# Kernel tuning notes

Measured on AMD Instinct MI355X. Metric: run time of the kernel, lower is better.

## Reference

```python
import jax, jax.numpy as jnp
from jax import lax
import numpy as np

B, NG, NC = 4, 513, 512  # batch, grid size N, coef size N-1

_STENCILS = [[[-1/6, 2/3], [-1/3, -1/6]],
             [[2/3, -1/6], [-1/6, -1/3]],
             [[-1/6, -1/3], [2/3, -1/6]],
             [[-1/3, -1/6], [-1/6, 2/3]]]

def _kernel():
    # torch: vstack 4 (1,1,2,2) kernels -> permute(1,0,2,3) => (out=1, in=4, 2, 2)
    return jnp.asarray(_STENCILS, jnp.float32)[None]

def darcy(x, a, kernel):
    # x: (B,1,N,N), a: (B,1,N-1,N-1)
    N = x.shape[-1]
    X = jnp.concatenate([x[:, :, 1:N, :N-1] * a,
                         x[:, :, 1:N, 1:] * a,
                         x[:, :, :N-1, 1:] * a,
                         x[:, :, :N-1, :N-1] * a], axis=1)  # (B,4,N-1,N-1)
    Ax = lax.conv_general_dilated(X, kernel, (1, 1), 'VALID')  # (B,1,N-2,N-2)
    return jnp.pad(Ax, ((0, 0), (0, 0), (1, 1), (1, 1)))

def _conv3(x, w):
    # x: (Cin,H,W), w: (Cout,Cin,3,3), padding=1
    return lax.conv_general_dilated(x[None], w, (1, 1), ((1, 1), (1, 1)))[0]
_CONVB = jax.vmap(_conv3)

def mcc(x, w):
    # per-sample complex 3x3 conv == torch multi_channel_conv diagonal trick
    yr = _CONVB(x.real, w.real) - _CONVB(x.imag, w.imag)
    yi = _CONVB(x.real, w.imag) + _CONVB(x.imag, w.real)
    return yr + 1j * yi

def conjT(w):
    # transpose(-4,-3).transpose(-2,-1).conj()
    return jnp.conj(jnp.swapaxes(jnp.swapaxes(w, 1, 2), -2, -1))

def expand(r):
    Bb, C, M, N = r.shape
    Z = jnp.zeros((Bb, C, 2 * (M + 1), 2 * (N + 1)), r.dtype)
    Z = Z.at[:, :, 1:M+1, 1:N+1].set(r)
    Z = Z.at[:, :, M+2:, 1:N+1].set(-r[:, :, ::-1, :])
    Z = Z.at[:, :, 1:M+1, N+2:].set(-r[:, :, :, ::-1])
    Z = Z.at[:, :, M+2:, N+2:].set(r[:, :, ::-1, ::-1])
    kg = jnp.arange(-M - 1, N + 1, dtype=jnp.float32) * jnp.float32(np.pi)
    ik2 = 1.0 / (kg[:, None] ** 2 + kg[None, :] ** 2)
    ik2 = ik2.at[M + 1, N + 1].set(1.0)
    N2 = 2 * (N + 1)
    lo = N2 // 2 - N2 // 4
    hi = N2 // 2 + N2 // 4 + 1
    return Z, ik2[lo:hi, lo:hi][None, None]

def H_apply(r, w1, w2, w3, wt):
    N1 = r.shape[-1]
    rsym, ik2 = expand(r)
    N2 = rsym.shape[-1]
    lo = N2 // 2 - N2 // 4
    hi = N2 // 2 + N2 // 4 + 1
    rh = jnp.fft.fftshift(jnp.fft.ifft2(rsym, axes=(2, 3)), axes=(2, 3))[:, :, lo:hi, lo:hi]
    for w in (w1, w2, w3):
        rh = mcc(rh, w)
    out = rh * wt * ik2
    for w in (conjT(w3), conjT(w2), conjT(w1)):
        out = mcc(out, w)
    pl = N2 // 4 + 1
    pr = N2 - N2 // 2 - pl
    out = jnp.pad(out, ((0, 0), (0, 0), (pl, pr), (pl, pr)))
    e = jnp.fft.fft2(jnp.fft.ifftshift(out, axes=(2, 3)), axes=(2, 3)).real
    return e[:, :, :N1, :N1]

def fns_step(x, f, a, dinv, kernel, ws):
    # Jacobi smoother, w=3/4, M=10
    for _ in range(10):
        r = f - darcy(x, a, kernel)
        x = x.at[:, :, 1:-1, 1:-1].add(0.75 * dinv * r[:, :, 1:-1, 1:-1])
    r = f - darcy(x, a, kernel)
    e = H_apply(r[:, :, 1:-1, 1:-1], *ws)
    e = jnp.pad(e, ((0, 0), (0, 0), (1, 1), (1, 1)))
    Ae = darcy(e, a, kernel)
    alpha = (jnp.sum(r * e, axis=(1, 2, 3)) / jnp.sum(Ae * e, axis=(1, 2, 3)))[:, None, None, None]
    return x + alpha * e

def _forward(f, coef, w1, w2, w3, wt, K):
    kernel = _kernel()
    diag_k = (2.0 / 3.0) * jnp.ones((1, 1, 2, 2), jnp.float32)
    dinv = 1.0 / lax.conv_general_dilated(coef, diag_k, (1, 1), 'VALID')
    ws = (w1, w2, w3, wt)
    x = jnp.zeros_like(f)
    for _ in range(K):
        x = fns_step(x, f, coef, dinv, kernel, ws)
    r = f - darcy(x, coef, kernel)
    return jnp.linalg.norm(r.reshape(-1)) / jnp.linalg.norm(f.reshape(-1))

def setup_inputs():
    key = jax.random.key(0)
    ks = jax.random.split(key, 12)
    s = jnp.float32(0.1)
    inp = {
        'f': jax.random.normal(ks[0], (B, 1, NG, NG), jnp.float32),
        'coef': jax.random.uniform(ks[1], (B, 1, NC, NC), jnp.float32) + 0.1,
        'u': jnp.zeros((B, 1, NG, NG), jnp.float32),
        'w1r': jax.random.normal(ks[2], (B, 4, 1, 3, 3), jnp.float32) * s,
        'w1i': jax.random.normal(ks[3], (B, 4, 1, 3, 3), jnp.float32) * s,
        'w2r': jax.random.normal(ks[4], (B, 4, 4, 3, 3), jnp.float32) * s,
        'w2i': jax.random.normal(ks[5], (B, 4, 4, 3, 3), jnp.float32) * s,
        'w3r': jax.random.normal(ks[6], (B, 1, 4, 3, 3), jnp.float32) * s,
        'w3i': jax.random.normal(ks[7], (B, 1, 4, 3, 3), jnp.float32) * s,
        'wtr': jax.random.normal(ks[8], (B, 1, NG, NG), jnp.float32) * s,
        'wti': jax.random.normal(ks[9], (B, 1, NG, NG), jnp.float32) * s,
        'epoch': 101,
    }
    return inp

def reference(f, coef, u, w1r, w1i, w2r, w2i, w3r, w3i, wtr, wti, epoch):
    K = (epoch - 1) // 100 + 1
    w1 = w1r + 1j * w1i
    w2 = w2r + 1j * w2i
    w3 = w3r + 1j * w3i
    wt = wtr + 1j * wti
    return _forward(f, coef, w1, w2, w3, wt, K)
```

## Files before the change

kernel.cpp:

```cpp
#include <hip/hip_runtime.h>
#include <math.h>

#ifndef M_PI
#define M_PI 3.14159265358979323846
#endif

#define NGRID 513
#define NCELL 512
#define NINT  511
#define NB    4

constexpr int N2G = NGRID * NGRID;
constexpr int NI2 = NINT * NINT;
constexpr int NTT = NGRID * NINT;

typedef unsigned short ushort;
typedef unsigned int uint32;
typedef __attribute__((ext_vector_type(8))) short short8;
typedef __attribute__((ext_vector_type(8))) unsigned short ushort8;
typedef __attribute__((ext_vector_type(4))) float f32x4;

__device__ __forceinline__ ushort f2bf(float x) {
    unsigned u = __float_as_uint(x);
    unsigned r = u + 0x7FFFu + ((u >> 16) & 1u);
    return (ushort)(r >> 16);
}
__device__ __forceinline__ float bf2f(ushort h) {
    return __uint_as_float(((unsigned)h) << 16);
}

__device__ __forceinline__ float darcyA(const float* __restrict__ x,
                                        const float* __restrict__ a,
                                        int i, int j) {
    const float c23 = 2.0f / 3.0f, c16 = 1.0f / 6.0f, c13 = 1.0f / 3.0f;
    float a00 = a[(i - 1) * NCELL + (j - 1)];
    float a01 = a[(i - 1) * NCELL + j];
    float a10 = a[i * NCELL + (j - 1)];
    float a11 = a[i * NCELL + j];
    const float* xm = x + (i - 1) * NGRID;
    const float* xc = x + i * NGRID;
    const float* xp = x + (i + 1) * NGRID;
    return c23 * (a00 + a01 + a10 + a11) * xc[j]
         - c16 * ((a00 + a01) * xm[j] + (a10 + a11) * xp[j]
                + (a00 + a10) * xc[j - 1] + (a01 + a11) * xc[j + 1])
         - c13 * (a00 * xm[j - 1] + a01 * xm[j + 1]
                + a10 * xp[j - 1] + a11 * xp[j + 1]);
}

__global__ void k_stencil(const float* __restrict__ xin,
                          const float* __restrict__ a,
                          const float* __restrict__ f,
                          const float* __restrict__ dinv,
                          float* __restrict__ out, int mode) {
    int b = blockIdx.z;
    int j = blockIdx.x * 16 + threadIdx.x;
    int i = blockIdx.y * 16 + threadIdx.y;
    if (i >= NGRID || j >= NGRID) return;
    const float* xb = xin + (long long)b * N2G;
    const float* ab = a + (long long)b * NCELL * NCELL;
    long long idx = (long long)b * N2G + (long long)i * NGRID + j;
    bool interior = (i >= 1 && i <= NINT && j >= 1 && j <= NINT);
    if (!interior) {
        out[idx] = (mode == 0) ? f[idx] : 0.0f;
        return;
    }
    float Ax = darcyA(xb, ab, i, j);
    if (mode == 0) {
        out[idx] = f[idx] - Ax;
    } else {
        out[idx] = Ax;
    }
}

__global__ void k_jacobi5(const float* __restrict__ xin,
                          const float* __restrict__ a,
                          const float* __restrict__ f,
                          const float* __restrict__ dinv,
                          float* __restrict__ out) {
    __shared__ float sx[26][26];
    __shared__ float sa[25][26];
    __shared__ float sf[24][24];
    __shared__ float sd[24][24];
    __shared__ float sp[2][24][26];
    const float c23 = 2.0f / 3.0f, c16 = 1.0f / 6.0f, c13 = 1.0f / 3.0f;
    int b = blockIdx.z;
    const float* xb = xin + (long long)b * N2G;
    const float* ab = a + (long long)b * NCELL * NCELL;
    const float* fb = f + (long long)b * N2G;
    const float* db = dinv + (long long)b * NI2;
    int ox = blockIdx.x * 16, oy = blockIdx.y * 16;
    int tx = threadIdx.x, ty = threadIdx.y;
    int tid = ty * 16 + tx;

    for (int idx = tid; idx < 26 * 26; idx += 256) {
        int ly = idx / 26, lx = idx % 26;
        int gy = oy - 5 + ly, gx = ox - 5 + lx;
        bool in = (gy >= 0 && gy < NGRID && gx >= 0 && gx < NGRID);
        sx[ly][lx] = in ? xb[(long long)gy * NGRID + gx] : 0.0f;
    }
    for (int idx = tid; idx < 25 * 25; idx += 256) {
        int ly = idx / 25, lx = idx % 25;
        int gy = oy - 5 + ly, gx = ox - 5 + lx;
        bool in = (gy >= 0 && gy < NCELL && gx >= 0 && gx < NCELL);
        sa[ly][lx] = in ? ab[(long long)gy * NCELL + gx] : 0.0f;
    }
    for (int idx = tid; idx < 24 * 24; idx += 256) {
        int ly = idx / 24, lx = idx % 24;
        int gy = oy - 4 + ly, gx = ox - 4 + lx;
        bool ing = (gy >= 0 && gy < NGRID && gx >= 0 && gx < NGRID);
        bool itr = (gy >= 1 && gy <= NINT && gx >= 1 && gx <= NINT);
        sf[ly][lx] = ing ? fb[(long long)gy * NGRID + gx] : 0.0f;
        sd[ly][lx] = itr ? db[(long long)(gy - 1) * NINT + (gx - 1)] : 0.0f;
    }
    __syncthreads();

    for (int idx = tid; idx < 24 * 24; idx += 256) {
        int ly = idx / 24, lx = idx % 24;
        int gy = oy - 4 + ly, gx = ox - 4 + lx;
        float v = 0.0f;
        if (gy >= 0 && gy < NGRID && gx >= 0 && gx < NGRID) {
            float xc = sx[ly + 1][lx + 1];
            if (gy >= 1 && gy <= NINT && gx >= 1 && gx <= NINT) {
                float a00 = sa[ly][lx], a01 = sa[ly][lx + 1];
                float a10 = sa[ly + 1][lx], a11 = sa[ly + 1][lx + 1];
                float Ax = c23 * (a00 + a01 + a10 + a11) * xc
                    - c16 * ((a00 + a01) * sx[ly][lx + 1] + (a10 + a11) * sx[ly + 2][lx + 1]
                           + (a00 + a10) * sx[ly + 1][lx] + (a01 + a11) * sx[ly + 1][lx + 2])
                    - c13 * (a00 * sx[ly][lx] + a01 * sx[ly][lx + 2]
                           + a10 * sx[ly + 2][lx] + a11 * sx[ly + 2][lx + 2]);
                v = xc + 0.75f * sd[ly][lx] * (sf[ly][lx] - Ax);
            } else {
                v = xc;
            }
        }
        sp[0][ly][lx] = v;
    }
    __syncthreads();

    #pragma unroll 1
    for (int s = 2; s <= 4; ++s) {
        int sz = 24 - 2 * (s - 1);
        int cur = (s - 1) & 1, prv = s & 1;
        for (int idx = tid; idx < sz * sz; idx += 256) {
            int ly = idx / sz, lx = idx % sz;
            int gy = oy - (5 - s) + ly, gx = ox - (5 - s) + lx;
            float v = 0.0f;
            if (gy >= 0 && gy < NGRID && gx >= 0 && gx < NGRID) {
                float xc = sp[prv][ly + 1][lx + 1];
                if (gy >= 1 && gy <= NINT && gx >= 1 && gx <= NINT) {
                    int ar = ly + s - 1, ac = lx + s - 1;
                    float a00 = sa[ar][ac], a01 = sa[ar][ac + 1];
                    float a10 = sa[ar + 1][ac], a11 = sa[ar + 1][ac + 1];
                    float Ax = c23 * (a00 + a01 + a10 + a11) * xc
                        - c16 * ((a00 + a01) * sp[prv][ly][lx + 1] + (a10 + a11) * sp[prv][ly + 2][lx + 1]
                               + (a00 + a10) * sp[prv][ly + 1][lx] + (a01 + a11) * sp[prv][ly + 1][lx + 2])
                        - c13 * (a00 * sp[prv][ly][lx] + a01 * sp[prv][ly][lx + 2]
                               + a10 * sp[prv][ly + 2][lx] + a11 * sp[prv][ly + 2][lx + 2]);
                    int fr = ly + s - 1, fc = lx + s - 1;
                    v = xc + 0.75f * sd[fr][fc] * (sf[fr][fc] - Ax);
                } else {
                    v = xc;
                }
            }
            sp[cur][ly][lx] = v;
        }
        __syncthreads();
    }

    {
        int gy = oy + ty, gx = ox + tx;
        if (gy < NGRID && gx < NGRID) {
            float v;
            float xc = sp[1][ty + 1][tx + 1];
            if (gy >= 1 && gy <= NINT && gx >= 1 && gx <= NINT) {
                int ar = ty + 4, ac = tx + 4;
                float a00 = sa[ar][ac], a01 = sa[ar][ac + 1];
                float a10 = sa[ar + 1][ac], a11 = sa[ar + 1][ac + 1];
                float Ax = c23 * (a00 + a01 + a10 + a11) * xc
                    - c16 * ((a00 + a01) * sp[1][ty][tx + 1] + (a10 + a11) * sp[1][ty + 2][tx + 1]
                           + (a00 + a10) * sp[1][ty + 1][tx] + (a01 + a11) * sp[1][ty + 1][tx + 2])
                    - c13 * (a00 * sp[1][ty][tx] + a01 * sp[1][ty][tx + 2]
                           + a10 * sp[1][ty + 2][tx] + a11 * sp[1][ty + 2][tx + 2]);
                v = xc + 0.75f * sd[ty + 4][tx + 4] * (sf[ty + 4][tx + 4] - Ax);
            } else {
                v = xc;
            }
            out[(long long)b * N2G + (long long)gy * NGRID + gx] = v;
        }
    }
}

__global__ void k_dinv(const float* __restrict__ a, float* __restrict__ dinv) {
    long long idx = (long long)blockIdx.x * blockDim.x + threadIdx.x;
    if (idx >= (long long)NB * NI2) return;
    int b = (int)(idx / NI2);
    int rem = (int)(idx % NI2);
    int p = rem / NINT, q = rem % NINT;
    const float* ab = a + (long long)b * NCELL * NCELL;
    float s = ab[p * NCELL + q] + ab[p * NCELL + q + 1]
            + ab[(p + 1) * NCELL + q] + ab[(p + 1) * NCELL + q + 1];
    dinv[idx] = 1.0f / ((2.0f / 3.0f) * s);
}

__device__ __forceinline__ void wsplit(double v, ushort* Dh, ushort* Dl, int idx) {
    float vf = (float)v;
    ushort h = f2bf(vf);
    Dh[idx] = h;
    Dl[idx] = f2bf(vf - bf2f(h));
}

__global__ void k_genDSTA(ushort* __restrict__ Dh, ushort* __restrict__ Dl) {
    int idx = blockIdx.x * 256 + threadIdx.x;
    if (idx >= 513 * 512) return;
    int u = idx / 512, k = idx % 512;
    double v = 0.0;
    if (k < 511) {
        int t = ((u - 256) * (k + 1)) % 1024;
        if (t < 0) t += 1024;
        v = sin((M_PI / 512.0) * (double)t);
    }
    wsplit(v, Dh, Dl, idx);
}

__global__ void k_genDSTB(ushort* __restrict__ Dh, ushort* __restrict__ Dl) {
    int idx = blockIdx.x * 256 + threadIdx.x;
    if (idx >= 513 * 512) return;
    int v = idx / 512, k = idx % 512;
    double val = 0.0;
    if (k < 511) {
        int t = ((v - 256) * (k + 1)) % 1024;
        if (t < 0) t += 1024;
        val = sin((M_PI / 512.0) * (double)t) * (-1.0 / 262144.0);
    }
    wsplit(val, Dh, Dl, idx);
}

__global__ void k_genFA(ushort* __restrict__ Dh, ushort* __restrict__ Dl) {
    int idx = blockIdx.x * 256 + threadIdx.x;
    if (idx >= 511 * 1056) return;
    int y = idx / 1056, k = idx % 1056;
    double v = 0.0;
    if (k < 1026) {
        int m = (k < 513) ? k : (k - 513);
        long t = ((long)y * (m - 255)) % 1025;
        if (t < 0) t += 1025;
        double ang = (2.0 * M_PI / 1025.0) * (double)t;
        v = (k < 513) ? cos(ang) : -sin(ang);
    }
    wsplit(v, Dh, Dl, idx);
}

__global__ void k_genFB(ushort* __restrict__ Dh, ushort* __restrict__ Dl) {
    int idx = blockIdx.x * 256 + threadIdx.x;
    if (idx >= 1022 * 1056) return;
    int n = idx / 1056, k = idx % 1056;
    double v = 0.0;
    if (k < 1026) {
        int m = (k < 513) ? k : (k - 513);
        int y = (n < 511) ? n : (n - 511);
        long t = ((long)y * (m - 255)) % 1025;
        if (t < 0) t += 1025;
        double ang = (2.0 * M_PI / 1025.0) * (double)t;
        bool ktop = (k < 513), nleft = (n < 511);
        if (ktop && nleft)        v = cos(ang);
        else if (ktop && !nleft)  v = -sin(ang);
        else if (!ktop && nleft)  v = sin(ang);
        else                      v = cos(ang);
    }
    wsplit(v, Dh, Dl, idx);
}

__global__ void k_cvtA(const float* __restrict__ s1, const float* __restrict__ s2,
                       long long bs1, long long bs2, int ld1, int ld2, int S,
                       int M, int K, int Kp,
                       ushort* __restrict__ Dh, ushort* __restrict__ Dl) {
    int b = blockIdx.y;
    int idx = blockIdx.x * 256 + threadIdx.x;
    if (idx >= M * Kp) return;
    int m = idx / Kp, k = idx % Kp;
    float v = 0.0f;
    if (k < K)
        v = (k < S) ? s1[b * bs1 + (long long)m * ld1 + k]
                    : s2[b * bs2 + (long long)m * ld2 + (k - S)];
    long long o = (long long)b * M * Kp + idx;
    ushort h = f2bf(v);
    Dh[o] = h;
    Dl[o] = f2bf(v - bf2f(h));
}

__global__ void k_cvtBt(const float* __restrict__ s1,
                        long long bs1, int ld1,
                        int N, int K, int Kp,
                        ushort* __restrict__ Dh, ushort* __restrict__ Dl) {
    int b = blockIdx.y;
    int idx = blockIdx.x * 256 + threadIdx.x;
    if (idx >= N * Kp) return;
    int n = idx / Kp, k = idx % Kp;
    float v = 0.0f;
    if (k < K)
        v = s1[b * bs1 + (long long)k * ld1 + n];
    long long o = (long long)b * N * Kp + idx;
    ushort h = f2bf(v);
    Dh[o] = h;
    Dl[o] = f2bf(v - bf2f(h));
}

__global__ void k_redA(const float* __restrict__ P, int nsplit,
                       ushort* __restrict__ Dh, ushort* __restrict__ Dl) {
    int b = blockIdx.y;
    int idx = blockIdx.x * 256 + threadIdx.x;
    if (idx >= 513 * 512) return;
    int m = idx / 512, k = idx % 512;
    float v = 0.0f;
    if (k < 511) {
        long long base = (long long)m * 511 + k;
        #pragma unroll 4
        for (int s = 0; s < nsplit; ++s)
            v += P[((long long)b * nsplit + s) * NTT + base];
    }
    long long o = (long long)b * 513 * 512 + idx;
    ushort h = f2bf(v);
    Dh[o] = h;
    Dl[o] = f2bf(v - bf2f(h));
}

__global__ void k_redBt(const float* __restrict__ P, int nsplit,
                        ushort* __restrict__ Dh, ushort* __restrict__ Dl) {
    int b = blockIdx.y;
    int idx = blockIdx.x * 256 + threadIdx.x;
    if (idx >= 511 * 1056) return;
    int n = idx / 1056, k = idx % 1056;
    float v = 0.0f;
    if (k < 1026) {
        int row = (k < 513) ? n : (511 + n);
        int col = (k < 513) ? k : (k - 513);
        long long base = (long long)row * 513 + col;
        float acc = 0.0f;
        #pragma unroll 4
        for (int s = 0; s < nsplit; ++s)
            acc += P[((long long)b * nsplit + s) * (1022LL * 513) + base];
        v = (k < 513) ? acc : -acc;
    }
    long long o = (long long)b * 511 * 1056 + idx;
    ushort h = f2bf(v);
    Dh[o] = h;
    Dl[o] = f2bf(v - bf2f(h));
}

__global__ __launch_bounds__(256) void k_mgemm(
    const ushort* __restrict__ Ah, const ushort* __restrict__ Al, long long bsA,
    const ushort* __restrict__ Bh, const ushort* __restrict__ Bl, long long bsB,
    float* __restrict__ C, long long bsC,
    int M, int N, int Kp, int nsplit) {
    __shared__ ushort sAh[128 * 40];
    __shared__ ushort sAl[128 * 40];
    __shared__ ushort sBh[128 * 40];
    __shared__ ushort sBl[128 * 40];

    int bz = blockIdx.z, b = bz / nsplit, ks = bz % nsplit;
    int kchunk = (((Kp + nsplit - 1) / nsplit) + 31) & ~31;
    int kbeg = ks * kchunk;
    int kend = min(Kp, kbeg + kchunk);

    Ah += b * bsA; Al += b * bsA;
    Bh += b * bsB; Bl += b * bsB;
    C += ((long long)b * nsplit + ks) * bsC;

    int bm = blockIdx.y * 128, bn = blockIdx.x * 128;
    int tid = threadIdx.x;
    int wave = tid >> 6, lane = tid & 63;
    int wm = (wave >> 1) * 64, wn = (wave & 1) * 64;
    int quad = lane >> 4, l16 = lane & 15;

    f32x4 zf = {0.f, 0.f, 0.f, 0.f};
    f32x4 acc[4][4];
    #pragma unroll
    for (int i = 0; i < 4; ++i)
        #pragma unroll
        for (int j = 0; j < 4; ++j) acc[i][j] = zf;

    int srow = tid >> 2;
    int sk8 = (tid & 3) * 8;

    for (int kt = kbeg; kt < kend; kt += 32) {
        #pragma unroll
        for (int h = 0; h < 2; ++h) {
            int row = srow + 64 * h;
            ushort8 vh = {0, 0, 0, 0, 0, 0, 0, 0};
            ushort8 vl = {0, 0, 0, 0, 0, 0, 0, 0};
            int gm = bm + row;
            if (gm < M) {
                vh = *(const ushort8*)(Ah + (long long)gm * Kp + kt + sk8);
                vl = *(const ushort8*)(Al + (long long)gm * Kp + kt + sk8);
            }
            *(ushort8*)(sAh + row * 40 + sk8) = vh;
            *(ushort8*)(sAl + row * 40 + sk8) = vl;
            ushort8 wh = {0, 0, 0, 0, 0, 0, 0, 0};
            ushort8 wl = {0, 0, 0, 0, 0, 0, 0, 0};
            int gn = bn + row;
            if (gn < N) {
                wh = *(const ushort8*)(Bh + (long long)gn * Kp + kt + sk8);
                wl = *(const ushort8*)(Bl + (long long)gn * Kp + kt + sk8);
            }
            *(ushort8*)(sBh + row * 40 + sk8) = wh;
            *(ushort8*)(sBl + row * 40 + sk8) = wl;
        }
        __syncthreads();

        short8 afh[4], afl[4], bfh[4], bfl[4];
        #pragma unroll
        for (int t = 0; t < 4; ++t) {
            int ar = wm + t * 16 + l16;
            afh[t] = *(const short8*)(sAh + ar * 40 + quad * 8);
            afl[t] = *(const short8*)(sAl + ar * 40 + quad * 8);
            int br = wn + t * 16 + l16;
            bfh[t] = *(const short8*)(sBh + br * 40 + quad * 8);
            bfl[t] = *(const short8*)(sBl + br * 40 + quad * 8);
        }
        #pragma unroll
        for (int mt = 0; mt < 4; ++mt)
            #pragma unroll
            for (int nt = 0; nt < 4; ++nt) {
                acc[mt][nt] = __builtin_amdgcn_mfma_f32_16x16x32_bf16(
                    afh[mt], bfh[nt], acc[mt][nt], 0, 0, 0);
                acc[mt][nt] = __builtin_amdgcn_mfma_f32_16x16x32_bf16(
                    afh[mt], bfl[nt], acc[mt][nt], 0, 0, 0);
                acc[mt][nt] = __builtin_amdgcn_mfma_f32_16x16x32_bf16(
                    afl[mt], bfh[nt], acc[mt][nt], 0, 0, 0);
            }
        __syncthreads();
    }

    #pragma unroll
    for (int mt = 0; mt < 4; ++mt) {
        #pragma unroll
        for (int r = 0; r < 4; ++r) {
            int gm = bm + wm + mt * 16 + quad * 4 + r;
            if (gm >= M) continue;
            long long rowoff = (long long)gm * N;
            #pragma unroll
            for (int nt = 0; nt < 4; ++nt) {
                int gn = bn + wn + nt * 16 + l16;
                if (gn < N) C[rowoff + gn] = acc[mt][nt][r];
            }
        }
    }
}

__global__ void k_reduce(const float* __restrict__ Pr,
                         float* __restrict__ outR,
                         int MN, int N, int ldo, long long bsOut, int nsplit) {
    int b = blockIdx.y;
    for (int idx = blockIdx.x * 256 + threadIdx.x; idx < MN;
         idx += gridDim.x * 256) {
        float sr = 0.0f;
        #pragma unroll 4
        for (int s = 0; s < nsplit; ++s)
            sr += Pr[((long long)b * nsplit + s) * MN + idx];
        int m = idx / N, n = idx - m * N;
        outR[(long long)b * bsOut + (long long)m * ldo + n] = sr;
    }
}

__device__ __forceinline__ float2 cmul(float2 a, float2 b) {
    return make_float2(a.x * b.x - a.y * b.y, a.x * b.y + a.y * b.x);
}

__global__ void k_compose(const float* __restrict__ w1r, const float* __restrict__ w1i,
                          const float* __restrict__ w2r, const float* __restrict__ w2i,
                          const float* __restrict__ w3r, const float* __restrict__ w3i,
                          float* __restrict__ kc) {
    int chain = blockIdx.x, b = blockIdx.y;
    int tid = threadIdx.x;
    __shared__ float2 sW1[4][9], sW2[16][9], sW3[4][9], sW21[4][25];
    for (int idx = tid; idx < 36; idx += 128) {
        int c = idx / 9, s = idx % 9, p = s / 3, q = s % 3;
        if (chain == 0) {
            int i1 = b * 36 + c * 9 + p * 3 + q;
            sW1[c][s] = make_float2(w1r[i1], w1i[i1]);
            sW3[c][s] = make_float2(w3r[i1], w3i[i1]);
        } else {
            int it = b * 36 + c * 9 + q * 3 + p;
            sW1[c][s] = make_float2(w3r[it], -w3i[it]);
            sW3[c][s] = make_float2(w1r[it], -w1i[it]);
        }
    }
    for (int idx = tid; idx < 144; idx += 128) {
        int co = idx / 36, r = idx % 36, ci = r / 9, s = r % 9, p = s / 3, q = s % 3;
        int iw = (chain == 0) ? (b * 144 + co * 36 + ci * 9 + p * 3 + q)
                              : (b * 144 + ci * 36 + co * 9 + q * 3 + p);
        float iv = w2i[iw];
        sW2[co * 4 + ci][s] = make_float2(w2r[iw], (chain == 0) ? iv : -iv);
    }
    __syncthreads();
    for (int idx = tid; idx < 100; idx += 128) {
        int cm = idx / 25, r = idx % 25, di = r / 5 - 2, dj = r % 5 - 2;
        float2 acc = make_float2(0.f, 0.f);
        for (int c1 = 0; c1 < 4; ++c1)
            for (int p = 0; p < 3; ++p)
                for (int q = 0; q < 3; ++q) {
                    int ei = di - (p - 1) + 1, ej = dj - (q - 1) + 1;
                    if (ei >= 0 && ei < 3 && ej >= 0 && ej < 3) {
                        float2 t = cmul(sW2[cm * 4 + c1][p * 3 + q], sW1[c1][ei * 3 + ej]);
                        acc.x += t.x; acc.y += t.y;
                    }
                }
        sW21[cm][r] = acc;
    }
    __syncthreads();
    for (int idx = tid; idx < 49; idx += 128) {
        int di = idx / 7 - 3, dj = idx % 7 - 3;
        float2 acc = make_float2(0.f, 0.f);
        for (int cm = 0; cm < 4; ++cm)
            for (int p = 0; p < 3; ++p)
                for (int q = 0; q < 3; ++q) {
                    int ei = di - (p - 1), ej = dj - (q - 1);
                    if (ei >= -2 && ei <= 2 && ej >= -2 && ej <= 2) {
                        float2 t = cmul(sW3[cm][p * 3 + q], sW21[cm][(ei + 2) * 5 + (ej + 2)]);
                        acc.x += t.x; acc.y += t.y;
                    }
                }
        ((float2*)kc)[(b * 2 + chain) * 49 + idx] = acc;
    }
}

template <bool CPLX>
__global__ __launch_bounds__(256) void k_conv7(
    const float* __restrict__ xr, const float* __restrict__ xi,
    const float* __restrict__ kc, int chain,
    float* __restrict__ outr, float* __restrict__ outi) {
    __shared__ float2 tile[134][23];
    __shared__ float2 kt[49];
    int b = blockIdx.z;
    int tid = threadIdx.y * 16 + threadIdx.x;
    const float2* kb = (const float2*)kc + (b * 2 + chain) * 49;
    for (int idx = tid; idx < 49; idx += 256) kt[idx] = kb[idx];
    int row_base = blockIdx.y * 128 - 3;
    int col_base = blockIdx.x * 16 - 3;
    for (int idx = tid; idx < 134 * 22; idx += 256) {
        int r = idx / 22, c = idx % 22;
        int gr = row_base + r, gc = col_base + c;
        bool in = (gr >= 0 && gr < NGRID && gc >= 0 && gc < NGRID);
        long long g = (long long)b * N2G + (long long)gr * NGRID + gc;
        float vr = in ? xr[g] : 0.0f;
        float vi = (CPLX && in) ? xi[g] : 0.0f;
        tile[r][c] = make_float2(vr, vi);
    }
    __syncthreads();

    int tx = threadIdx.x, r0 = threadIdx.y * 8;
    float2 acc[8];
    #pragma unroll
    for (int r = 0; r < 8; ++r) acc[r] = make_float2(0.f, 0.f);
    #pragma unroll
    for (int t = 0; t < 7; ++t) {
        float2 kv[7];
        #pragma unroll
        for (int s = 0; s < 7; ++s) kv[s] = kt[s * 7 + t];
        #pragma unroll
        for (int rr = 0; rr < 14; ++rr) {
            float2 xv = tile[r0 + rr][tx + t];
            #pragma unroll
            for (int s = 0; s < 7; ++s) {
                int orow = rr - s;
                if (orow >= 0 && orow < 8) {
                    acc[orow].x += kv[s].x * xv.x;
                    acc[orow].y += kv[s].y * xv.x;
                    if (CPLX) {
                        acc[orow].x -= kv[s].y * xv.y;
                        acc[orow].y += kv[s].x * xv.y;
                    }
                }
            }
        }
    }
    int gc = blockIdx.x * 16 + tx;
    if (gc >= NGRID) return;
    #pragma unroll
    for (int r = 0; r < 8; ++r) {
        int gr = blockIdx.y * 128 + r0 + r;
        if (gr < NGRID) {
            long long g = (long long)b * N2G + (long long)gr * NGRID + gc;
            outr[g] = acc[r].x;
            outi[g] = acc[r].y;
        }
    }
}

template <int CHAIN>
__global__ __launch_bounds__(256) void k_ring7(
    const float* __restrict__ xr, const float* __restrict__ xi,
    const float* __restrict__ w1r, const float* __restrict__ w1i,
    const float* __restrict__ w2r, const float* __restrict__ w2i,
    const float* __restrict__ w3r, const float* __restrict__ w3i,
    float* __restrict__ outr, float* __restrict__ outi) {
    constexpr bool CPLX = (CHAIN == 1);
    __shared__ float2 W1s[4][9], W2s[16][9], W3s[4][9];
    __shared__ float2 Y[4][4][68];
    __shared__ float2 Z[4][3][66];
    int side = blockIdx.y, b = blockIdx.z;
    int u0 = blockIdx.x * 64;
    int ulo = (side < 2) ? 0 : 2;
    int uhi = (side < 2) ? (NGRID - 1) : (NGRID - 3);
    if (u0 > uhi) return;
    int tid = threadIdx.x;

    for (int idx = tid; idx < 36; idx += 256) {
        int c = idx / 9, s = idx % 9, p = s / 3, q = s % 3;
        if (CHAIN == 0) {
            int i1 = b * 36 + c * 9 + p * 3 + q;
            W1s[c][s] = make_float2(w1r[i1], w1i[i1]);
            W3s[c][s] = make_float2(w3r[i1], w3i[i1]);
        } else {
            int it = b * 36 + c * 9 + q * 3 + p;
            W1s[c][s] = make_float2(w3r[it], -w3i[it]);
            W3s[c][s] = make_float2(w1r[it], -w1i[it]);
        }
    }
    for (int idx = tid; idx < 144; idx += 256) {
        int co = idx / 36, r = idx % 36, ci = r / 9, s = r % 9, p = s / 3, q = s % 3;
        int iw = (CHAIN == 0) ? (b * 144 + co * 36 + ci * 9 + p * 3 + q)
                              : (b * 144 + ci * 36 + co * 9 + q * 3 + p);
        float iv = w2i[iw];
        W2s[co * 4 + ci][s] = make_float2(w2r[iw], (CHAIN == 0) ? iv : -iv);
    }
    __syncthreads();

    for (int idx = tid; idx < 4 * 4 * 68; idx += 256) {
        int ch = idx / (4 * 68), r = idx % (4 * 68), d = r / 68, uu = r % 68;
        int u = u0 - 2 + uu;
        float2 acc = make_float2(0.f, 0.f);
        if (u >= 0 && u < NGRID) {
            int i, j;
            if (side == 0)      { i = d;       j = u; }
            else if (side == 1) { i = 512 - d; j = u; }
            else if (side == 2) { i = u;       j = d; }
            else                { i = u;       j = 512 - d; }
            for (int p = 0; p < 3; ++p)
                for (int q = 0; q < 3; ++q) {
                    int ii = i + p - 1, jj = j + q - 1;
                    if (ii >= 0 && ii < NGRID && jj >= 0 && jj < NGRID) {
                        long long g = (long long)b * N2G + (long long)ii * NGRID + jj;
                        float vr = xr[g];
                        float vi = CPLX ? xi[g] : 0.0f;
                        float2 w = W1s[ch][p * 3 + q];
                        acc.x += w.x * vr - w.y * vi;
                        acc.y += w.x * vi + w.y * vr;
                    }
                }
        }
        Y[ch][d][uu] = acc;
    }
    __syncthreads();

    for (int idx = tid; idx < 4 * 3 * 66; idx += 256) {
        int co = idx / (3 * 66), r = idx % (3 * 66), d = r / 66, uu = r % 66;
        int u = u0 - 1 + uu;
        float2 acc = make_float2(0.f, 0.f);
        if (u >= 0 && u < NGRID) {
            for (int p = 0; p < 3; ++p)
                for (int q = 0; q < 3; ++q) {
                    int dd, du;
                    if (side == 0)      { dd = p - 1; du = q - 1; }
                    else if (side == 1) { dd = 1 - p; du = q - 1; }
                    else if (side == 2) { dd = q - 1; du = p - 1; }
                    else                { dd = 1 - q; du = p - 1; }
                    int d2 = d + dd, uy = uu + 1 + du;
                    if (d2 >= 0) {
                        for (int ci = 0; ci < 4; ++ci) {
                            float2 yv = Y[ci][d2][uy];
                            float2 w = W2s[co * 4 + ci][p * 3 + q];
                            acc.x += w.x * yv.x - w.y * yv.y;
                            acc.y += w.x * yv.y + w.y * yv.x;
                        }
                    }
                }
        }
        Z[co][d][uu] = acc;
    }
    __syncthreads();

    for (int idx = tid; idx < 128; idx += 256) {
        int d = idx / 64, uu = idx % 64;
        int u = u0 + uu;
        if (u < ulo || u > uhi) continue;
        float2 acc = make_float2(0.f, 0.f);
        for (int p = 0; p < 3; ++p)
            for (int q = 0; q < 3; ++q) {
                int dd, du;
                if (side == 0)      { dd = p - 1; du = q - 1; }
                else if (side == 1) { dd = 1 - p; du = q - 1; }
                else if (side == 2) { dd = q - 1; du = p - 1; }
                else                { dd = 1 - q; du = p - 1; }
                int d2 = d + dd, uz = uu + 1 + du;
                if (d2 >= 0) {
                    for (int ci = 0; ci < 4; ++ci) {
                        float2 zv = Z[ci][d2][uz];
                        float2 w = W3s[ci][p * 3 + q];
                        acc.x += w.x * zv.x - w.y * zv.y;
                        acc.y += w.x * zv.y + w.y * zv.x;
                    }
                }
            }
        int i, j;
        if (side == 0)      { i = d;       j = u; }
        else if (side == 1) { i = 512 - d; j = u; }
        else if (side == 2) { i = u;       j = d; }
        else                { i = u;       j = 512 - d; }
        long long g = (long long)b * N2G + (long long)i * NGRID + j;
        outr[g] = acc.x;
        outi[g] = acc.y;
    }
}

__global__ void k_scale(float* __restrict__ or_, float* __restrict__ oi_,
                        const float* __restrict__ wtr, const float* __restrict__ wti) {
    long long idx = (long long)blockIdx.x * blockDim.x + threadIdx.x;
    if (idx >= (long long)NB * N2G) return;
    int pix = (int)(idx % N2G);
    int u = pix / NGRID, v = pix % NGRID;
    int du = u - 256, dv = v - 256;
    float ik2;
    if (du == 0 && dv == 0)
        ik2 = 1.0f;
    else
        ik2 = (float)(1.0 / (9.869604401089358 * (double)(du * du + dv * dv)));
    float xr = or_[idx], xv = oi_[idx];
    float wrv = wtr[idx], wiv = wti[idx];
    or_[idx] = (xr * wrv - xv * wiv) * ik2;
    oi_[idx] = (xr * wiv + xv * wrv) * ik2;
}

__global__ void k_dot2(const float* __restrict__ r, const float* __restrict__ e,
                       const float* __restrict__ Ae, float* __restrict__ red) {
    int b = blockIdx.y;
    const float* rb = r + (long long)b * N2G;
    const float* eb = e + (long long)b * N2G;
    const float* ab = Ae + (long long)b * N2G;
    float s1 = 0.0f, s2 = 0.0f;
    for (int i = blockIdx.x * blockDim.x + threadIdx.x; i < N2G;
         i += gridDim.x * blockDim.x) {
        float ev = eb[i];
        s1 += rb[i] * ev;
        s2 += ab[i] * ev;
    }
    #pragma unroll
    for (int o = 32; o > 0; o >>= 1) {
        s1 += __shfl_down(s1, o);
        s2 += __shfl_down(s2, o);
    }
    __shared__ float l1[4], l2[4];
    int wid = threadIdx.x >> 6;
    if ((threadIdx.x & 63) == 0) { l1[wid] = s1; l2[wid] = s2; }
    __syncthreads();
    if (threadIdx.x == 0) {
        atomicAdd(&red[2 * b], l1[0] + l1[1] + l1[2] + l1[3]);
        atomicAdd(&red[2 * b + 1], l2[0] + l2[1] + l2[2] + l2[3]);
    }
}

__global__ void k_update(float* __restrict__ x, const float* __restrict__ e,
                         const float* __restrict__ red) {
    long long idx = (long long)blockIdx.x * blockDim.x + threadIdx.x;
    if (idx >= (long long)NB * N2G) return;
    int b = (int)(idx / N2G);
    float alpha = red[2 * b] / red[2 * b + 1];
    x[idx] += alpha * e[idx];
}

__global__ void k_norm(const float* __restrict__ r, const float* __restrict__ f,
                       float* __restrict__ red) {
    float s1 = 0.0f, s2 = 0.0f;
    for (long long i = (long long)blockIdx.x * blockDim.x + threadIdx.x;
         i < (long long)NB * N2G; i += (long long)gridDim.x * blockDim.x) {
        float rv = r[i], fv = f[i];
        s1 += rv * rv;
        s2 += fv * fv;
    }
    #pragma unroll
    for (int o = 32; o > 0; o >>= 1) {
        s1 += __shfl_down(s1, o);
        s2 += __shfl_down(s2, o);
    }
    __shared__ float l1[4], l2[4];
    int wid = threadIdx.x >> 6;
    if ((threadIdx.x & 63) == 0) { l1[wid] = s1; l2[wid] = s2; }
    __syncthreads();
    if (threadIdx.x == 0) {
        atomicAdd(&red[8], l1[0] + l1[1] + l1[2] + l1[3]);
        atomicAdd(&red[9], l2[0] + l2[1] + l2[2] + l2[3]);
    }
}

__global__ void k_final(const float* __restrict__ red, float* __restrict__ out) {
    out[0] = sqrtf(red[8] / red[9]);
}

extern "C" void kernel_launch(void* const* d_in, const int* in_sizes, int n_in,
                              void* d_out, int out_size, void* d_ws, size_t ws_size,
                              hipStream_t stream) {
    (void)in_sizes; (void)n_in; (void)out_size; (void)ws_size;
    const float* f    = (const float*)d_in[0];
    const float* coef = (const float*)d_in[1];
    const float* w1r  = (const float*)d_in[3];
    const float* w1i  = (const float*)d_in[4];
    const float* w2r  = (const float*)d_in[5];
    const float* w2i  = (const float*)d_in[6];
    const float* w3r  = (const float*)d_in[7];
    const float* w3i  = (const float*)d_in[8];
    const float* wtr  = (const float*)d_in[9];
    const float* wti  = (const float*)d_in[10];
    float* out = (float*)d_out;

    float* ws = (float*)d_ws;
    size_t off = 0;
    auto alloc = [&](long long n) {
        float* p = ws + off;
        off += (size_t)((n + 3) & ~3LL);
        return p;
    };
    float* x0   = alloc((long long)NB * N2G);
    float* x1   = alloc((long long)NB * N2G);
    float* rr   = alloc((long long)NB * N2G);
    float* ee   = alloc((long long)NB * N2G);
    float* rh   = alloc((long long)NB * N2G);
    float* dinv = alloc((long long)NB * NI2);
    float* c1r  = alloc((long long)NB * 4 * N2G);
    float* c1i  = alloc((long long)NB * 4 * N2G);
    float* c2r  = alloc((long long)NB * 4 * N2G);
    float* c2i  = alloc((long long)NB * 4 * N2G);
    float* pr   = c1r;
    float* or_  = alloc((long long)NB * N2G);
    float* oi_  = alloc((long long)NB * N2G);
    float* red  = alloc(16);
    ushort* sGh  = (ushort*)alloc(513 * 512 / 2);
    ushort* sGl  = (ushort*)alloc(513 * 512 / 2);
    ushort* sGth = (ushort*)alloc(513 * 512 / 2);
    ushort* sGtl = (ushort*)alloc(513 * 512 / 2);
    ushort* sFAh = (ushort*)alloc(511 * 1056 / 2);
    ushort* sFAl = (ushort*)alloc(511 * 1056 / 2);
    ushort* sFBh = (ushort*)alloc(1022 * 1056 / 2);
    ushort* sFBl = (ushort*)alloc(1022 * 1056 / 2);
    ushort* dAh  = (ushort*)alloc((long long)NB * 513 * 1056 / 2);
    ushort* dAl  = (ushort*)alloc((long long)NB * 513 * 1056 / 2);
    ushort* dBh  = (ushort*)alloc((long long)NB * 511 * 1056 / 2);
    ushort* dBl  = (ushort*)alloc((long long)NB * 511 * 1056 / 2);
    float* kcomp = alloc(NB * 2 * 49 * 2);
    float* Ae   = rh;

    dim3 blk2(16, 16);
    dim3 grdS(33, 33, NB);
    dim3 grdC(33, 5, NB);
    dim3 grdR(9, 4, NB);
    const int SP = 4;

    hipMemsetAsync(x0, 0, (size_t)NB * N2G * sizeof(float), stream);
    k_dinv<<<dim3((NB * NI2 + 255) / 256), dim3(256), 0, stream>>>(coef, dinv);
    k_genDSTA<<<dim3((513 * 512 + 255) / 256), dim3(256), 0, stream>>>(sGh, sGl);
    k_genDSTB<<<dim3((513 * 512 + 255) / 256), dim3(256), 0, stream>>>(sGth, sGtl);
    k_genFA<<<dim3((511 * 1056 + 255) / 256), dim3(256), 0, stream>>>(sFAh, sFAl);
    k_genFB<<<dim3((1022 * 1056 + 255) / 256), dim3(256), 0, stream>>>(sFBh, sFBl);
    k_compose<<<dim3(2, NB), dim3(128), 0, stream>>>(w1r, w1i, w2r, w2i, w3r, w3i, kcomp);

    float* xa = x0;
    float* xb = x1;
    for (int step = 0; step < 2; ++step) {
        for (int it = 0; it < 2; ++it) {
            k_jacobi5<<<grdS, blk2, 0, stream>>>(xa, coef, f, dinv, xb);
            float* t = xa; xa = xb; xb = t;
        }
        k_stencil<<<grdS, blk2, 0, stream>>>(xa, coef, f, nullptr, rr, 0);

        k_cvtBt<<<dim3((511 * 512 + 255) / 256, NB), dim3(256), 0, stream>>>(
            rr + NGRID + 1, N2G, NGRID, 511, 511, 512, dBh, dBl);
        k_mgemm<<<dim3(4, 5, NB * SP), dim3(256), 0, stream>>>(
            sGh, sGl, 0, dBh, dBl, (long long)511 * 512,
            pr, (long long)NTT, 513, 511, 512, SP);
        k_redA<<<dim3(1026, NB), dim3(256), 0, stream>>>(pr, SP, dAh, dAl);
        k_mgemm<<<dim3(5, 5, NB * SP), dim3(256), 0, stream>>>(
            dAh, dAl, (long long)513 * 512, sGth, sGtl, 0,
            pr, (long long)N2G, 513, 513, 512, SP);
        k_reduce<<<dim3(1024, NB), dim3(256), 0, stream>>>(
            pr, rh, N2G, NGRID, NGRID, (long long)N2G, SP);

        k_conv7<false><<<grdC, blk2, 0, stream>>>(rh, nullptr, kcomp, 0, or_, oi_);
        k_ring7<0><<<grdR, dim3(256), 0, stream>>>(
            rh, nullptr, w1r, w1i, w2r, w2i, w3r, w3i, or_, oi_);
        k_scale<<<dim3((NB * N2G + 255) / 256), dim3(256), 0, stream>>>(or_, oi_, wtr, wti);
        k_conv7<true><<<grdC, blk2, 0, stream>>>(or_, oi_, kcomp, 1, c1r, c1i);
        k_ring7<1><<<grdR, dim3(256), 0, stream>>>(
            or_, oi_, w1r, w1i, w2r, w2i, w3r, w3i, c1r, c1i);

        k_cvtA<<<dim3((513 * 1056 + 255) / 256, NB), dim3(256), 0, stream>>>(
            c1r, c1i, N2G, N2G, NGRID, NGRID, 513, 513, 1026, 1056, dAh, dAl);
        k_mgemm<<<dim3(5, 8, NB * 4), dim3(256), 0, stream>>>(
            sFBh, sFBl, 0, dAh, dAl, (long long)513 * 1056,
            pr, 1022LL * 513, 1022, 513, 1056, 4);
        k_redBt<<<dim3(2109, NB), dim3(256), 0, stream>>>(pr, 4, dBh, dBl);
        k_mgemm<<<dim3(4, 4, NB * SP), dim3(256), 0, stream>>>(
            sFAh, sFAl, 0, dBh, dBl, (long long)511 * 1056,
            pr, (long long)NI2, 511, 511, 1056, SP);
        hipMemsetAsync(ee, 0, (size_t)NB * N2G * sizeof(float), stream);
        k_reduce<<<dim3(1024, NB), dim3(256), 0, stream>>>(
            pr, ee + NGRID + 1, NI2, NINT, NGRID, (long long)N2G, SP);

        k_stencil<<<grdS, blk2, 0, stream>>>(ee, coef, nullptr, nullptr, Ae, 2);
        hipMemsetAsync(red, 0, 8 * sizeof(float), stream);
        k_dot2<<<dim3(64, NB), dim3(256), 0, stream>>>(rr, ee, Ae, red);
        k_update<<<dim3((NB * N2G + 255) / 256), dim3(256), 0, stream>>>(xa, ee, red);
    }
    k_stencil<<<grdS, blk2, 0, stream>>>(xa, coef, f, nullptr, rr, 0);
    hipMemsetAsync(red + 8, 0, 2 * sizeof(float), stream);
    k_norm<<<dim3(256), dim3(256), 0, stream>>>(rr, f, red);
    k_final<<<dim3(1), dim3(1), 0, stream>>>(red, out);
}
```

Before: 752.0 us.

## Exploit spectral odd symmetry to compute quarter transform; fuse conversions into producers

The forward spectral transform now produces only a 257x257 quadrant, and consumers rebuild the full 513x513 field from it through a sign-flipping symmetric read. This shrinks both forward GEMMs and the reduction. The bf16 hi/lo split conversion of the residual is fused into the stencil kernel through a shared-memory transpose. The wavenumber scaling and the bf16 packing of the conv outputs are fused into conv7 and ring7, which removes the separate scale and cvtA/cvtBt passes and their global round trips. The cost is extra per-element index logic and scaling work in the conv loads, plus added memsets to zero the padded bf16 buffers.

```diff
diff --git a/kernel.cpp b/kernel.cpp
--- a/kernel.cpp
+++ b/kernel.cpp
@@ -12,7 +12,7 @@
 
 constexpr int N2G = NGRID * NGRID;
 constexpr int NI2 = NINT * NINT;
-constexpr int NTT = NGRID * NINT;
+constexpr int NQ  = 257 * 257;
 
 typedef unsigned short ushort;
 typedef unsigned int uint32;
@@ -27,6 +27,25 @@
 }
 __device__ __forceinline__ float bf2f(ushort h) {
     return __uint_as_float(((unsigned)h) << 16);
+}
+
+__device__ __forceinline__ float rhq_read(const float* __restrict__ rq,
+                                          int i, int j) {
+    float s = 1.0f;
+    if (i > 256) { i = 512 - i; s = -s; }
+    if (j > 256) { j = 512 - j; s = -s; }
+    return s * rq[i * 257 + j];
+}
+
+__device__ __forceinline__ float2 scale_wt(float x0, float x1, float wr, float wi,
+                                           int gr, int gc) {
+    int du = gr - 256, dv = gc - 256;
+    float ik2;
+    if (du == 0 && dv == 0)
+        ik2 = 1.0f;
+    else
+        ik2 = (float)(1.0 / (9.869604401089358 * (double)(du * du + dv * dv)));
+    return make_float2((x0 * wr - x1 * wi) * ik2, (x0 * wi + x1 * wr) * ik2);
 }
 
 __device__ __forceinline__ float darcyA(const float* __restrict__ x,
@@ -50,25 +69,39 @@
 __global__ void k_stencil(const float* __restrict__ xin,
                           const float* __restrict__ a,
                           const float* __restrict__ f,
-                          const float* __restrict__ dinv,
-                          float* __restrict__ out, int mode) {
+                          float* __restrict__ out, int mode,
+                          ushort* __restrict__ tBh, ushort* __restrict__ tBl) {
+    __shared__ float st[16][17];
     int b = blockIdx.z;
     int j = blockIdx.x * 16 + threadIdx.x;
     int i = blockIdx.y * 16 + threadIdx.y;
-    if (i >= NGRID || j >= NGRID) return;
     const float* xb = xin + (long long)b * N2G;
     const float* ab = a + (long long)b * NCELL * NCELL;
+    bool ingrid = (i < NGRID && j < NGRID);
+    bool interior = ingrid && i >= 1 && i <= NINT && j >= 1 && j <= NINT;
+    float v = 0.0f;
     long long idx = (long long)b * N2G + (long long)i * NGRID + j;
-    bool interior = (i >= 1 && i <= NINT && j >= 1 && j <= NINT);
-    if (!interior) {
-        out[idx] = (mode == 0) ? f[idx] : 0.0f;
-        return;
-    }
-    float Ax = darcyA(xb, ab, i, j);
-    if (mode == 0) {
-        out[idx] = f[idx] - Ax;
-    } else {
-        out[idx] = Ax;
+    if (interior) {
+        float Ax = darcyA(xb, ab, i, j);
+        v = (mode == 0) ? f[idx] - Ax : Ax;
+    } else if (ingrid) {
+        v = (mode == 0) ? f[idx] : 0.0f;
+    }
+    if (ingrid) out[idx] = v;
+    if (mode == 0 && tBh) {
+        st[threadIdx.y][threadIdx.x] = v;
+        __syncthreads();
+        int tx = threadIdx.x, ty = threadIdx.y;
+        int i2 = blockIdx.y * 16 + tx;
+        int j2 = blockIdx.x * 16 + ty;
+        if (i2 >= 1 && i2 <= NINT && j2 >= 1 && j2 <= NINT) {
+            float rv = st[tx][ty];
+            ushort h = f2bf(rv);
+            long long o = (long long)b * 511 * 512
+                        + (long long)(j2 - 1) * 512 + (i2 - 1);
+            tBh[o] = h;
+            tBl[o] = f2bf(rv - bf2f(h));
+        }
     }
 }
 
@@ -270,55 +303,21 @@
     wsplit(v, Dh, Dl, idx);
 }
 
-__global__ void k_cvtA(const float* __restrict__ s1, const float* __restrict__ s2,
-                       long long bs1, long long bs2, int ld1, int ld2, int S,
-                       int M, int K, int Kp,
+__global__ void k_redA(const float* __restrict__ P, int nsplit, int Mr,
                        ushort* __restrict__ Dh, ushort* __restrict__ Dl) {
     int b = blockIdx.y;
     int idx = blockIdx.x * 256 + threadIdx.x;
-    if (idx >= M * Kp) return;
-    int m = idx / Kp, k = idx % Kp;
-    float v = 0.0f;
-    if (k < K)
-        v = (k < S) ? s1[b * bs1 + (long long)m * ld1 + k]
-                    : s2[b * bs2 + (long long)m * ld2 + (k - S)];
-    long long o = (long long)b * M * Kp + idx;
-    ushort h = f2bf(v);
-    Dh[o] = h;
-    Dl[o] = f2bf(v - bf2f(h));
-}
-
-__global__ void k_cvtBt(const float* __restrict__ s1,
-                        long long bs1, int ld1,
-                        int N, int K, int Kp,
-                        ushort* __restrict__ Dh, ushort* __restrict__ Dl) {
-    int b = blockIdx.y;
-    int idx = blockIdx.x * 256 + threadIdx.x;
-    if (idx >= N * Kp) return;
-    int n = idx / Kp, k = idx % Kp;
-    float v = 0.0f;
-    if (k < K)
-        v = s1[b * bs1 + (long long)k * ld1 + n];
-    long long o = (long long)b * N * Kp + idx;
-    ushort h = f2bf(v);
-    Dh[o] = h;
-    Dl[o] = f2bf(v - bf2f(h));
-}
-
-__global__ void k_redA(const float* __restrict__ P, int nsplit,
-                       ushort* __restrict__ Dh, ushort* __restrict__ Dl) {
-    int b = blockIdx.y;
-    int idx = blockIdx.x * 256 + threadIdx.x;
-    if (idx >= 513 * 512) return;
+    if (idx >= Mr * 512) return;
     int m = idx / 512, k = idx % 512;
     float v = 0.0f;
     if (k < 511) {
         long long base = (long long)m * 511 + k;
+        long long str = (long long)Mr * 511;
         #pragma unroll 4
         for (int s = 0; s < nsplit; ++s)
-            v += P[((long long)b * nsplit + s) * NTT + base];
-    }
-    long long o = (long long)b * 513 * 512 + idx;
+            v += P[((long long)b * nsplit + s) * str + base];
+    }
+    long long o = (long long)b * Mr * 512 + idx;
     ushort h = f2bf(v);
     Dh[o] = h;
     Dl[o] = f2bf(v - bf2f(h));
@@ -524,26 +523,36 @@
     }
 }
 
-template <bool CPLX>
+template <int MODE>
 __global__ __launch_bounds__(256) void k_conv7(
     const float* __restrict__ xr, const float* __restrict__ xi,
-    const float* __restrict__ kc, int chain,
-    float* __restrict__ outr, float* __restrict__ outi) {
+    const float* __restrict__ wtr, const float* __restrict__ wti,
+    const float* __restrict__ kc,
+    float* __restrict__ outr, float* __restrict__ outi,
+    ushort* __restrict__ oAh, ushort* __restrict__ oAl) {
+    constexpr bool CPLX = (MODE == 1);
     __shared__ float2 tile[134][23];
     __shared__ float2 kt[49];
     int b = blockIdx.z;
     int tid = threadIdx.y * 16 + threadIdx.x;
-    const float2* kb = (const float2*)kc + (b * 2 + chain) * 49;
+    const float2* kb = (const float2*)kc + (b * 2 + MODE) * 49;
     for (int idx = tid; idx < 49; idx += 256) kt[idx] = kb[idx];
     int row_base = blockIdx.y * 128 - 3;
     int col_base = blockIdx.x * 16 - 3;
+    const float* rq = xr + (long long)b * NQ;
     for (int idx = tid; idx < 134 * 22; idx += 256) {
         int r = idx / 22, c = idx % 22;
         int gr = row_base + r, gc = col_base + c;
-        bool in = (gr >= 0 && gr < NGRID && gc >= 0 && gc < NGRID);
-        long long g = (long long)b * N2G + (long long)gr * NGRID + gc;
-        float vr = in ? xr[g] : 0.0f;
-        float vi = (CPLX && in) ? xi[g] : 0.0f;
+        float vr = 0.0f, vi = 0.0f;
+        if (gr >= 0 && gr < NGRID && gc >= 0 && gc < NGRID) {
+            if (MODE == 0) {
+                vr = rhq_read(rq, gr, gc);
+            } else {
+                long long g = (long long)b * N2G + (long long)gr * NGRID + gc;
+                float2 sc = scale_wt(xr[g], xi[g], wtr[g], wti[g], gr, gc);
+                vr = sc.x; vi = sc.y;
+            }
+        }
         tile[r][c] = make_float2(vr, vi);
     }
     __syncthreads();
@@ -580,9 +589,20 @@
     for (int r = 0; r < 8; ++r) {
         int gr = blockIdx.y * 128 + r0 + r;
         if (gr < NGRID) {
-            long long g = (long long)b * N2G + (long long)gr * NGRID + gc;
-            outr[g] = acc[r].x;
-            outi[g] = acc[r].y;
+            if (MODE == 0) {
+                long long g = (long long)b * N2G + (long long)gr * NGRID + gc;
+                outr[g] = acc[r].x;
+                outi[g] = acc[r].y;
+            } else {
+                long long o = (long long)b * 513 * 1056
+                            + (long long)gr * 1056 + gc;
+                ushort h = f2bf(acc[r].x);
+                oAh[o] = h;
+                oAl[o] = f2bf(acc[r].x - bf2f(h));
+                ushort h2 = f2bf(acc[r].y);
+                oAh[o + 513] = h2;
+                oAl[o + 513] = f2bf(acc[r].y - bf2f(h2));
+            }
         }
     }
 }
@@ -590,10 +610,12 @@
 template <int CHAIN>
 __global__ __launch_bounds__(256) void k_ring7(
     const float* __restrict__ xr, const float* __restrict__ xi,
+    const float* __restrict__ wtr, const float* __restrict__ wti,
     const float* __restrict__ w1r, const float* __restrict__ w1i,
     const float* __restrict__ w2r, const float* __restrict__ w2i,
     const float* __restrict__ w3r, const float* __restrict__ w3i,
-    float* __restrict__ outr, float* __restrict__ outi) {
+    float* __restrict__ outr, float* __restrict__ outi,
+    ushort* __restrict__ oAh, ushort* __restrict__ oAl) {
     constexpr bool CPLX = (CHAIN == 1);
     __shared__ float2 W1s[4][9], W2s[16][9], W3s[4][9];
     __shared__ float2 Y[4][4][68];
@@ -604,6 +626,7 @@
     int uhi = (side < 2) ? (NGRID - 1) : (NGRID - 3);
     if (u0 > uhi) return;
     int tid = threadIdx.x;
+    const float* rq = xr + (long long)b * NQ;
 
     for (int idx = tid; idx < 36; idx += 256) {
         int c = idx / 9, s = idx % 9, p = s / 3, q = s % 3;
@@ -640,9 +663,17 @@
                 for (int q = 0; q < 3; ++q) {
                     int ii = i + p - 1, jj = j + q - 1;
                     if (ii >= 0 && ii < NGRID && jj >= 0 && jj < NGRID) {
-                        long long g = (long long)b * N2G + (long long)ii * NGRID + jj;
-                        float vr = xr[g];
-                        float vi = CPLX ? xi[g] : 0.0f;
+                        float vr, vi;
+                        if (CHAIN == 0) {
+                            vr = rhq_read(rq, ii, jj);
+                            vi = 0.0f;
+                        } else {
+                            long long g = (long long)b * N2G
+                                        + (long long)ii * NGRID + jj;
+                            float2 sc = scale_wt(xr[g], xi[g], wtr[g], wti[g],
+                                                 ii, jj);
+                            vr = sc.x; vi = sc.y;
+                        }
                         float2 w = W1s[ch][p * 3 + q];
                         acc.x += w.x * vr - w.y * vi;
                         acc.y += w.x * vi + w.y * vr;
@@ -707,28 +738,20 @@
         else if (side == 1) { i = 512 - d; j = u; }
         else if (side == 2) { i = u;       j = d; }
         else                { i = u;       j = 512 - d; }
-        long long g = (long long)b * N2G + (long long)i * NGRID + j;
-        outr[g] = acc.x;
-        outi[g] = acc.y;
-    }
-}
-
-__global__ void k_scale(float* __restrict__ or_, float* __restrict__ oi_,
-                        const float* __restrict__ wtr, const float* __restrict__ wti) {
-    long long idx = (long long)blockIdx.x * blockDim.x + threadIdx.x;
-    if (idx >= (long long)NB * N2G) return;
-    int pix = (int)(idx % N2G);
-    int u = pix / NGRID, v = pix % NGRID;
-    int du = u - 256, dv = v - 256;
-    float ik2;
-    if (du == 0 && dv == 0)
-        ik2 = 1.0f;
-    else
-        ik2 = (float)(1.0 / (9.869604401089358 * (double)(du * du + dv * dv)));
-    float xr = or_[idx], xv = oi_[idx];
-    float wrv = wtr[idx], wiv = wti[idx];
-    or_[idx] = (xr * wrv - xv * wiv) * ik2;
-    oi_[idx] = (xr * wiv + xv * wrv) * ik2;
+        if (CHAIN == 0) {
+            long long g = (long long)b * N2G + (long long)i * NGRID + j;
+            outr[g] = acc.x;
+            outi[g] = acc.y;
+        } else {
+            long long o = (long long)b * 513 * 1056 + (long long)i * 1056 + j;
+            ushort h = f2bf(acc.x);
+            oAh[o] = h;
+            oAl[o] = f2bf(acc.x - bf2f(h));
+            ushort h2 = f2bf(acc.y);
+            oAh[o + 513] = h2;
+            oAl[o + 513] = f2bf(acc.y - bf2f(h2));
+        }
+    }
 }
 
 __global__ void k_dot2(const float* __restrict__ r, const float* __restrict__ e,
@@ -823,7 +846,6 @@
     float* x1   = alloc((long long)NB * N2G);
     float* rr   = alloc((long long)NB * N2G);
     float* ee   = alloc((long long)NB * N2G);
-    float* rh   = alloc((long long)NB * N2G);
     float* dinv = alloc((long long)NB * NI2);
     float* c1r  = alloc((long long)NB * 4 * N2G);
     float* c1i  = alloc((long long)NB * 4 * N2G);
@@ -832,6 +854,7 @@
     float* pr   = c1r;
     float* or_  = alloc((long long)NB * N2G);
     float* oi_  = alloc((long long)NB * N2G);
+    float* rhq  = alloc((long long)NB * NQ);
     float* red  = alloc(16);
     ushort* sGh  = (ushort*)alloc(513 * 512 / 2);
     ushort* sGl  = (ushort*)alloc(513 * 512 / 2);
@@ -841,12 +864,16 @@
     ushort* sFAl = (ushort*)alloc(511 * 1056 / 2);
     ushort* sFBh = (ushort*)alloc(1022 * 1056 / 2);
     ushort* sFBl = (ushort*)alloc(1022 * 1056 / 2);
-    ushort* dAh  = (ushort*)alloc((long long)NB * 513 * 1056 / 2);
-    ushort* dAl  = (ushort*)alloc((long long)NB * 513 * 1056 / 2);
-    ushort* dBh  = (ushort*)alloc((long long)NB * 511 * 1056 / 2);
-    ushort* dBl  = (ushort*)alloc((long long)NB * 511 * 1056 / 2);
+    ushort* dA2h = (ushort*)alloc((long long)NB * 257 * 512 / 2);
+    ushort* dA2l = (ushort*)alloc((long long)NB * 257 * 512 / 2);
+    ushort* dA3h = (ushort*)alloc((long long)NB * 513 * 1056 / 2);
+    ushort* dA3l = (ushort*)alloc((long long)NB * 513 * 1056 / 2);
+    ushort* dB1h = (ushort*)alloc((long long)NB * 511 * 512 / 2);
+    ushort* dB1l = (ushort*)alloc((long long)NB * 511 * 512 / 2);
+    ushort* dB4h = (ushort*)alloc((long long)NB * 511 * 1056 / 2);
+    ushort* dB4l = (ushort*)alloc((long long)NB * 511 * 1056 / 2);
     float* kcomp = alloc(NB * 2 * 49 * 2);
-    float* Ae   = rh;
+    float* Ae   = or_;
 
     dim3 blk2(16, 16);
     dim3 grdS(33, 33, NB);
@@ -855,6 +882,8 @@
     const int SP = 4;
 
     hipMemsetAsync(x0, 0, (size_t)NB * N2G * sizeof(float), stream);
+    hipMemsetAsync(dA3h, 0, (size_t)NB * 513 * 1056 * 2 * 2, stream);
+    hipMemsetAsync(dB1h, 0, (size_t)NB * 511 * 512 * 2 * 2, stream);
     k_dinv<<<dim3((NB * NI2 + 255) / 256), dim3(256), 0, stream>>>(coef, dinv);
     k_genDSTA<<<dim3((513 * 512 + 255) / 256), dim3(256), 0, stream>>>(sGh, sGl);
     k_genDSTB<<<dim3((513 * 512 + 255) / 256), dim3(256), 0, stream>>>(sGth, sGtl);
@@ -869,47 +898,48 @@
             k_jacobi5<<<grdS, blk2, 0, stream>>>(xa, coef, f, dinv, xb);
             float* t = xa; xa = xb; xb = t;
         }
-        k_stencil<<<grdS, blk2, 0, stream>>>(xa, coef, f, nullptr, rr, 0);
-
-        k_cvtBt<<<dim3((511 * 512 + 255) / 256, NB), dim3(256), 0, stream>>>(
-            rr + NGRID + 1, N2G, NGRID, 511, 511, 512, dBh, dBl);
-        k_mgemm<<<dim3(4, 5, NB * SP), dim3(256), 0, stream>>>(
-            sGh, sGl, 0, dBh, dBl, (long long)511 * 512,
-            pr, (long long)NTT, 513, 511, 512, SP);
-        k_redA<<<dim3(1026, NB), dim3(256), 0, stream>>>(pr, SP, dAh, dAl);
-        k_mgemm<<<dim3(5, 5, NB * SP), dim3(256), 0, stream>>>(
-            dAh, dAl, (long long)513 * 512, sGth, sGtl, 0,
-            pr, (long long)N2G, 513, 513, 512, SP);
-        k_reduce<<<dim3(1024, NB), dim3(256), 0, stream>>>(
-            pr, rh, N2G, NGRID, NGRID, (long long)N2G, SP);
-
-        k_conv7<false><<<grdC, blk2, 0, stream>>>(rh, nullptr, kcomp, 0, or_, oi_);
+        k_stencil<<<grdS, blk2, 0, stream>>>(xa, coef, f, rr, 0, dB1h, dB1l);
+
+        k_mgemm<<<dim3(4, 3, NB * SP), dim3(256), 0, stream>>>(
+            sGh, sGl, 0, dB1h, dB1l, (long long)511 * 512,
+            pr, (long long)257 * 511, 257, 511, 512, SP);
+        k_redA<<<dim3((257 * 512 + 255) / 256, NB), dim3(256), 0, stream>>>(
+            pr, SP, 257, dA2h, dA2l);
+        k_mgemm<<<dim3(3, 3, NB * SP), dim3(256), 0, stream>>>(
+            dA2h, dA2l, (long long)257 * 512, sGth, sGtl, 0,
+            pr, (long long)NQ, 257, 257, 512, SP);
+        k_reduce<<<dim3(259, NB), dim3(256), 0, stream>>>(
+            pr, rhq, NQ, 257, 257, (long long)NQ, SP);
+
+        k_conv7<0><<<grdC, blk2, 0, stream>>>(
+            rhq, nullptr, nullptr, nullptr, kcomp, or_, oi_, nullptr, nullptr);
         k_ring7<0><<<grdR, dim3(256), 0, stream>>>(
-            rh, nullptr, w1r, w1i, w2r, w2i, w3r, w3i, or_, oi_);
-        k_scale<<<dim3((NB * N2G + 255) / 256), dim3(256), 0, stream>>>(or_, oi_, wtr, wti);
-        k_conv7<true><<<grdC, blk2, 0, stream>>>(or_, oi_, kcomp, 1, c1r, c1i);
+            rhq, nullptr, nullptr, nullptr,
+            w1r, w1i, w2r, w2i, w3r, w3i, or_, oi_, nullptr, nullptr);
+        k_conv7<1><<<grdC, blk2, 0, stream>>>(
+            or_, oi_, wtr, wti, kcomp, nullptr, nullptr, dA3h, dA3l);
         k_ring7<1><<<grdR, dim3(256), 0, stream>>>(
-            or_, oi_, w1r, w1i, w2r, w2i, w3r, w3i, c1r, c1i);
-
-        k_cvtA<<<dim3((513 * 1056 + 255) / 256, NB), dim3(256), 0, stream>>>(
-            c1r, c1i, N2G, N2G, NGRID, NGRID, 513, 513, 1026, 1056, dAh, dAl);
+            or_, oi_, wtr, wti,
+            w1r, w1i, w2r, w2i, w3r, w3i, nullptr, nullptr, dA3h, dA3l);
+
         k_mgemm<<<dim3(5, 8, NB * 4), dim3(256), 0, stream>>>(
-            sFBh, sFBl, 0, dAh, dAl, (long long)513 * 1056,
+            sFBh, sFBl, 0, dA3h, dA3l, (long long)513 * 1056,
             pr, 1022LL * 513, 1022, 513, 1056, 4);
-        k_redBt<<<dim3(2109, NB), dim3(256), 0, stream>>>(pr, 4, dBh, dBl);
+        k_redBt<<<dim3(2109, NB), dim3(256), 0, stream>>>(pr, 4, dB4h, dB4l);
         k_mgemm<<<dim3(4, 4, NB * SP), dim3(256), 0, stream>>>(
-            sFAh, sFAl, 0, dBh, dBl, (long long)511 * 1056,
+            sFAh, sFAl, 0, dB4h, dB4l, (long long)511 * 1056,
             pr, (long long)NI2, 511, 511, 1056, SP);
         hipMemsetAsync(ee, 0, (size_t)NB * N2G * sizeof(float), stream);
         k_reduce<<<dim3(1024, NB), dim3(256), 0, stream>>>(
             pr, ee + NGRID + 1, NI2, NINT, NGRID, (long long)N2G, SP);
 
-        k_stencil<<<grdS, blk2, 0, stream>>>(ee, coef, nullptr, nullptr, Ae, 2);
+        k_stencil<<<grdS, blk2, 0, stream>>>(ee, coef, nullptr, Ae, 2,
+                                             nullptr, nullptr);
         hipMemsetAsync(red, 0, 8 * sizeof(float), stream);
         k_dot2<<<dim3(64, NB), dim3(256), 0, stream>>>(rr, ee, Ae, red);
         k_update<<<dim3((NB * N2G + 255) / 256), dim3(256), 0, stream>>>(xa, ee, red);
     }
-    k_stencil<<<grdS, blk2, 0, stream>>>(xa, coef, f, nullptr, rr, 0);
+    k_stencil<<<grdS, blk2, 0, stream>>>(xa, coef, f, rr, 0, nullptr, nullptr);
     hipMemsetAsync(red + 8, 0, 2 * sizeof(float), stream);
     k_norm<<<dim3(256), dim3(256), 0, stream>>>(rr, f, red);
     k_final<<<dim3(1), dim3(1), 0, stream>>>(red, out);
```

Result: faster. 721.0 us (-4.1%).
